# Kernel optimization log

Hardware: AMD Instinct MI355X
Metric: run time of the kernel (lower is better)

Reference implementation:

```python
import jax, jax.numpy as jnp
import numpy as np

# Qwen3.5 GatedDeltaNet dims
B, T, HID = 2, 2048, 2048
HK, HV, DK, DV, KW = 16, 32, 128, 128, 4   # k-heads, v-heads, head dims, conv kernel
R = HV // HK                                # GQA repeat factor = 2
KEY_DIM = HK * DK                           # 2048
VAL_DIM = HV * DV                           # 4096
CONV_DIM = 2 * KEY_DIM + VAL_DIM            # 8192
EPS = 1e-6


def setup_inputs() -> dict:
    key = jax.random.key(0)
    ks = jax.random.split(key, 10)
    w = lambda k, shape, s=0.02: (jax.random.normal(k, shape) * s).astype(jnp.float32)
    A = jax.random.uniform(ks[8], (HV,), minval=1e-3, maxval=16.0)
    return {
        "hidden_states": jax.random.normal(ks[0], (B, T, HID), jnp.float32),
        "W_qkv": w(ks[1], (HID, CONV_DIM)),
        "W_z": w(ks[2], (HID, VAL_DIM)),
        "W_b": w(ks[3], (HID, HV)),
        "W_a": w(ks[4], (HID, HV)),
        "conv_w": w(ks[5], (CONV_DIM, KW), 0.5),   # depthwise causal conv taps
        "dt_bias": jnp.ones((HV,), jnp.float32),
        "A_log": jnp.log(A).astype(jnp.float32),
        "norm_weight": jnp.ones((DV,), jnp.float32),
        "W_out": w(ks[9], (VAL_DIM, HID)),
    }


def _forward(hidden_states, W_qkv, W_z, W_b, W_a, conv_w, dt_bias, A_log, norm_weight, W_out):
    x = hidden_states
    # --- projections ---
    qkv = x @ W_qkv                                    # [B,T,CONV_DIM]
    z = x @ W_z                                        # [B,T,VAL_DIM]
    beta = jax.nn.sigmoid(x @ W_b)                     # [B,T,HV]
    alpha = x @ W_a                                    # [B,T,HV]
    g = -jnp.exp(A_log) * jax.nn.softplus(alpha + dt_bias)  # [B,T,HV] (log-decay <= 0)

    # --- fix_query_key_value_ordering: per-k-head interleaved layout ---
    qkv = qkv.reshape(B, T, HK, 2 * DK + R * DV)
    q, k, v = jnp.split(qkv, [DK, 2 * DK], axis=3)
    mixed = jnp.concatenate([q.reshape(B, T, -1), k.reshape(B, T, -1), v.reshape(B, T, -1)], axis=-1)

    # --- causal depthwise short conv (kernel 4) + SiLU ---
    xp = jnp.pad(mixed, ((0, 0), (KW - 1, 0), (0, 0)))
    conv = sum(conv_w[:, i] * xp[:, i:i + T, :] for i in range(KW))
    conv = jax.nn.silu(conv)

    q, k, v = jnp.split(conv, [KEY_DIM, 2 * KEY_DIM], axis=-1)
    q = q.reshape(B, T, HK, DK)
    k = k.reshape(B, T, HK, DK)
    v = v.reshape(B, T, HV, DV)
    gate = z.reshape(B, T, HV, DV)

    # GQA: repeat q,k heads to match v heads
    q = jnp.repeat(q, R, axis=2)                       # [B,T,HV,DK]
    k = jnp.repeat(k, R, axis=2)

    # l2-norm q,k (use_qk_l2norm_in_kernel=True) and default scale 1/sqrt(DK)
    q = q / jnp.sqrt(jnp.sum(q * q, axis=-1, keepdims=True) + 1e-6)
    k = k / jnp.sqrt(jnp.sum(k * k, axis=-1, keepdims=True) + 1e-6)
    q = q * (DK ** -0.5)

    # --- gated delta rule recurrence (scan over time) ---
    # state S: [B,HV,DK,DV];  S_t = a_t*S_{t-1} + k_t (beta_t*(v_t - (a_t*S_{t-1})^T k_t))^T
    def step(S, inp):
        qt, kt, vt, gt, bt = inp                       # [B,HV,DK],[B,HV,DK],[B,HV,DV],[B,HV],[B,HV]
        S = S * jnp.exp(gt)[:, :, None, None]
        kv = jnp.einsum('bhk,bhkv->bhv', kt, S)
        delta = bt[..., None] * (vt - kv)              # [B,HV,DV]
        S = S + kt[..., None] * delta[:, :, None, :]
        o = jnp.einsum('bhk,bhkv->bhv', qt, S)
        return S, o

    tfirst = lambda a: jnp.moveaxis(a, 1, 0)           # [T,B,...]
    S0 = jnp.zeros((B, HV, DK, DV), q.dtype)
    _, o = jax.lax.scan(step, S0, (tfirst(q), tfirst(k), tfirst(v), tfirst(g), tfirst(beta)))
    o = jnp.moveaxis(o, 0, 1)                          # [B,T,HV,DV]

    # --- gated RMSNorm: rmsnorm(o) * silu(gate) * weight ---
    var = jnp.mean(o * o, axis=-1, keepdims=True)
    o = o * jax.lax.rsqrt(var + EPS)
    o = o * jax.nn.silu(gate)
    o = o * norm_weight

    return o.reshape(B, T, VAL_DIM) @ W_out            # [B,T,HID]


def reference(hidden_states, W_qkv, W_z, W_b, W_a, conv_w, dt_bias, A_log, norm_weight, W_out):
    return _forward(hidden_states, W_qkv, W_z, W_b, W_a, conv_w, dt_bias, A_log, norm_weight, W_out)
```

## Files before the change

kernel.cpp:

```cpp
#include <hip/hip_runtime.h>


#define T_LEN 2048
#define MROWS 4096

typedef __bf16 bf16x8 __attribute__((ext_vector_type(8)));
typedef float f32x4 __attribute__((ext_vector_type(4)));

#define MFMA(a, b, c) __builtin_amdgcn_mfma_f32_16x16x32_bf16((a), (b), (c), 0, 0, 0)

__device__ __forceinline__ unsigned short f2bf(float f) {
  unsigned int u = __float_as_uint(f);
  unsigned int r = (u + 0x7fffu + ((u >> 16) & 1u)) >> 16;
  return (unsigned short)r;
}
__device__ __forceinline__ float bf2f(unsigned short u) {
  return __uint_as_float(((unsigned int)u) << 16);
}
__device__ __forceinline__ void gload_lds16(const void* g, void* l) {
  __builtin_amdgcn_global_load_lds(
      (const __attribute__((address_space(1))) unsigned int*)g,
      (__attribute__((address_space(3))) unsigned int*)l, 16, 0, 0);
}

__global__ __launch_bounds__(256) void f32_to_bf16_vec(const float* __restrict__ src,
                                                       unsigned short* __restrict__ dst,
                                                       int n4) {
  int i = blockIdx.x * 256 + threadIdx.x;
  if (i >= n4) return;
  float4 v = ((const float4*)src)[i];
  ushort4 o;
  o.x = f2bf(v.x); o.y = f2bf(v.y); o.z = f2bf(v.z); o.w = f2bf(v.w);
  ((ushort4*)dst)[i] = o;
}

__global__ __launch_bounds__(256) void transpose_f2b(const float* __restrict__ src,
                                                     unsigned short* __restrict__ dst,
                                                     int R, int C) {
  __shared__ float tile[32][33];
  int tx = threadIdx.x & 31, ty = threadIdx.x >> 5;
  int c0 = blockIdx.x * 32, r0 = blockIdx.y * 32;
  #pragma unroll
  for (int i = ty; i < 32; i += 8)
    tile[i][tx] = src[(size_t)(r0 + i) * C + c0 + tx];
  __syncthreads();
  #pragma unroll
  for (int i = ty; i < 32; i += 8)
    dst[(size_t)(c0 + i) * R + r0 + tx] = f2bf(tile[tx][i]);
}

template <int OUTBF, int BN>
__global__ __launch_bounds__(512, 2) void gemm256(const unsigned short* __restrict__ A, int lda,
                                                  const unsigned short* __restrict__ Bt, int ldb,
                                                  void* __restrict__ Cv, int ldc,
                                                  int M, int N, int K) {
  constexpr int BUFSZ = 16384 + BN * 64;
  constexpr int BISS = BN / 64;
  constexpr int IS = 4 + BISS;
  constexpr int WMv = (BN == 256) ? 2 : 4;
  constexpr int MSUB = 256 / (WMv * 16);
  constexpr int MSPAN = 256 / WMv;

  __shared__ unsigned short lds[2 * BUFSZ];

  const int mtiles = M >> 8;
  const int nwg = gridDim.x;
  const int orig = blockIdx.x;
  const int q = nwg >> 3, r = nwg & 7;
  const int xcd = orig & 7, idx = orig >> 3;
  const int swz = (xcd < r ? xcd * (q + 1) : r * (q + 1) + (xcd - r) * q) + idx;
  const int m0 = (swz % mtiles) * 256;
  const int n0 = (swz / mtiles) * BN;

  const int tid = threadIdx.x, lane = tid & 63, wv = tid >> 6;
  const int wm = (BN == 256) ? (wv >> 2) : (wv >> 1);
  const int wn = (BN == 256) ? (wv & 3) : (wv & 1);
  const int l15 = lane & 15, l4 = lane >> 4;

  f32x4 acc[MSUB][4];
  #pragma unroll
  for (int i = 0; i < MSUB; i++)
    #pragma unroll
    for (int j = 0; j < 4; j++) acc[i][j] = f32x4{0.f, 0.f, 0.f, 0.f};

  const int NT = K >> 6;

  auto STAGE = [&](int kt) {
    unsigned short* base = lds + (kt & 1) * BUFSZ;
    const int k0 = kt << 6;
    #pragma unroll
    for (int is = 0; is < 4; is++) {
      int ow = is * 8192 + wv * 1024;
      int o = ow + lane * 16;
      int row = o >> 7, colB = o & 127;
      int scol = colB ^ ((row & 7) << 4);
      gload_lds16(A + (size_t)(m0 + row) * lda + k0 + (scol >> 1), base + (ow >> 1));
    }
    #pragma unroll
    for (int is = 0; is < BISS; is++) {
      int ow = is * 8192 + wv * 1024;
      int o = ow + lane * 16;
      int row = o >> 7, colB = o & 127;
      int scol = colB ^ ((row & 7) << 4);
      gload_lds16(Bt + (size_t)(n0 + row) * ldb + k0 + (scol >> 1), base + 16384 + (ow >> 1));
    }
  };

  STAGE(0);
  if (NT > 1) STAGE(1);
  if constexpr (IS == 8) asm volatile("s_waitcnt vmcnt(8)" ::: "memory");
  else                   asm volatile("s_waitcnt vmcnt(6)" ::: "memory");
  __builtin_amdgcn_sched_barrier(0);
  __builtin_amdgcn_s_barrier();
  __builtin_amdgcn_sched_barrier(0);

  for (int t = 0; t < NT; t++) {
    const unsigned short* Abuf = lds + (t & 1) * BUFSZ;
    const unsigned short* Bbuf = Abuf + 16384;
    bf16x8 bF[4][2];
    #pragma unroll
    for (int n = 0; n < 4; n++) {
      int rb = wn * 64 + n * 16 + l15;
      int sw = (rb & 7) << 4;
      #pragma unroll
      for (int ks = 0; ks < 2; ks++) {
        int colB = (ks * 32 + l4 * 8) * 2;
        bF[n][ks] = *(const bf16x8*)(Bbuf + rb * 64 + ((colB ^ sw) >> 1));
      }
    }
    __builtin_amdgcn_s_setprio(1);
    #pragma unroll
    for (int m = 0; m < MSUB; m++) {
      int ra = wm * MSPAN + m * 16 + l15;
      int sw = (ra & 7) << 4;
      int c0b = l4 * 16;
      bf16x8 a0 = *(const bf16x8*)(Abuf + ra * 64 + ((c0b ^ sw) >> 1));
      bf16x8 a1 = *(const bf16x8*)(Abuf + ra * 64 + (((64 + c0b) ^ sw) >> 1));
      #pragma unroll
      for (int n = 0; n < 4; n++) {
        acc[m][n] = MFMA(a0, bF[n][0], acc[m][n]);
        acc[m][n] = MFMA(a1, bF[n][1], acc[m][n]);
      }
    }
    __builtin_amdgcn_s_setprio(0);
    __builtin_amdgcn_sched_barrier(0);
    __builtin_amdgcn_s_barrier();
    __builtin_amdgcn_sched_barrier(0);
    if (t + 2 < NT) STAGE(t + 2);
    if (t + 1 < NT) {
      if (t + 2 < NT) {
        if constexpr (IS == 8) asm volatile("s_waitcnt vmcnt(8)" ::: "memory");
        else                   asm volatile("s_waitcnt vmcnt(6)" ::: "memory");
      } else {
        asm volatile("s_waitcnt vmcnt(0)" ::: "memory");
      }
      __builtin_amdgcn_sched_barrier(0);
      __builtin_amdgcn_s_barrier();
      __builtin_amdgcn_sched_barrier(0);
    }
  }

  #pragma unroll
  for (int m = 0; m < MSUB; m++) {
    int grow = m0 + wm * MSPAN + m * 16 + l4 * 4;
    #pragma unroll
    for (int n = 0; n < 4; n++) {
      int gcol = n0 + wn * 64 + n * 16 + l15;
      if (OUTBF) {
        unsigned short* cp = (unsigned short*)Cv + (size_t)grow * ldc + gcol;
        #pragma unroll
        for (int rr = 0; rr < 4; rr++) cp[(size_t)rr * ldc] = f2bf(acc[m][n][rr]);
      } else {
        float* cp = (float*)Cv + (size_t)grow * ldc + gcol;
        #pragma unroll
        for (int rr = 0; rr < 4; rr++) cp[(size_t)rr * ldc] = acc[m][n][rr];
      }
    }
  }
}

template <int OUTBF>
__global__ __launch_bounds__(256) void gemm_bf16(const unsigned short* __restrict__ A, int lda,
                                                 const unsigned short* __restrict__ Bt, int ldb,
                                                 void* __restrict__ Cv, int ldc,
                                                 int M, int N, int K) {
  __shared__ unsigned short As[128 * 64];
  __shared__ unsigned short Bs[128 * 64];
  const int tid = threadIdx.x, lane = tid & 63, wv = tid >> 6;
  const int wr = wv >> 1, wc = wv & 1;
  const int m0 = blockIdx.y * 128, n0 = blockIdx.x * 128;
  const int lrow8 = lane >> 3;
  const int lk8 = (lane & 7) * 8;

  f32x4 acc[4][4];
  #pragma unroll
  for (int i = 0; i < 4; i++)
    #pragma unroll
    for (int j = 0; j < 4; j++) acc[i][j] = f32x4{0.f, 0.f, 0.f, 0.f};

  for (int k0 = 0; k0 < K; k0 += 64) {
    #pragma unroll
    for (int j = 0; j < 4; ++j) {
      int chunk = j * 4 + wv;
      int r = chunk * 8 + lrow8;
      gload_lds16(A + (size_t)(m0 + r) * lda + k0 + lk8, (void*)(As + chunk * 512));
      gload_lds16(Bt + (size_t)(n0 + r) * ldb + k0 + lk8, (void*)(Bs + chunk * 512));
    }
    __syncthreads();
    #pragma unroll
    for (int half = 0; half < 2; ++half) {
      int ko = half * 32 + (lane >> 4) * 8;
      bf16x8 af[4], bfr[4];
      #pragma unroll
      for (int i = 0; i < 4; i++) {
        int ra = wr * 64 + i * 16 + (lane & 15);
        af[i] = *(const bf16x8*)(As + ra * 64 + ko);
        int rb = wc * 64 + i * 16 + (lane & 15);
        bfr[i] = *(const bf16x8*)(Bs + rb * 64 + ko);
      }
      #pragma unroll
      for (int i = 0; i < 4; i++)
        #pragma unroll
        for (int j = 0; j < 4; j++)
          acc[i][j] = MFMA(af[i], bfr[j], acc[i][j]);
    }
    __syncthreads();
  }
  int cr4 = (lane >> 4) * 4;
  int cc = lane & 15;
  #pragma unroll
  for (int i = 0; i < 4; i++) {
    int row = m0 + wr * 64 + i * 16 + cr4;
    #pragma unroll
    for (int j = 0; j < 4; j++) {
      int col = n0 + wc * 64 + j * 16 + cc;
      if (OUTBF) {
        unsigned short* cp = (unsigned short*)Cv + (size_t)row * ldc + col;
        #pragma unroll
        for (int r = 0; r < 4; r++) cp[(size_t)r * ldc] = f2bf(acc[i][j][r]);
      } else {
        float* cp = (float*)Cv + (size_t)row * ldc + col;
        #pragma unroll
        for (int r = 0; r < 4; r++) cp[(size_t)r * ldc] = acc[i][j][r];
      }
    }
  }
}

__global__ __launch_bounds__(256) void beta_g_kernel(const unsigned short* __restrict__ ba,
                                                     const float* __restrict__ A_log,
                                                     const float* __restrict__ dt_bias,
                                                     unsigned short* __restrict__ betab,
                                                     float* __restrict__ g) {
  int i = blockIdx.x * 256 + threadIdx.x;
  int row = i >> 5, hv = i & 31;
  float rb = bf2f(ba[(size_t)row * 128 + hv]);
  float ra = bf2f(ba[(size_t)row * 128 + 32 + hv]);
  betab[i] = f2bf(1.f / (1.f + expf(-rb)));
  float xg = ra + dt_bias[hv];
  float sp = (xg > 20.f) ? xg : log1pf(expf(xg));
  g[i] = -expf(A_log[hv]) * sp;
}

__global__ __launch_bounds__(256) void conv_kernel(const unsigned short* __restrict__ qkv,
                                                   const float* __restrict__ conv_w,
                                                   unsigned short* __restrict__ out) {
  const int seg = blockIdx.x, tt = blockIdx.y, b = blockIdx.z;
  const int tid = threadIdx.x;
  const int c0 = seg * 128;
  const bool isq = seg < 16;
  int scb;
  if (isq) scb = seg * 512;
  else if (seg < 32) scb = (seg - 16) * 512 + 128;
  else scb = ((seg - 32) >> 1) * 512 + 256 + ((seg - 32) & 1) * 128;

  __shared__ unsigned short raw[35][136];
  __shared__ float cw[4][132];

  for (int i = tid; i < 512; i += 256) {
    int cl = i >> 2, tap = i & 3;
    cw[tap][cl] = conv_w[(size_t)(c0 + cl) * 4 + tap];
  }
  const int t0 = tt * 32;
  for (int i = tid; i < 560; i += 256) {
    int row = i >> 4, col = (i & 15) * 8;
    int gt = t0 - 3 + row;
    uint4 v = make_uint4(0u, 0u, 0u, 0u);
    if (gt >= 0) v = *(const uint4*)(qkv + (size_t)(b * T_LEN + gt) * 8192 + scb + col);
    *(uint4*)(&raw[row][col]) = v;
  }
  __syncthreads();
  const int s = tid >> 3, dg = tid & 7;
  union RawU { uint4 v[2]; unsigned short h[16]; };
  RawU u[4];
  #pragma unroll
  for (int i = 0; i < 4; i++) {
    const uint4* p = (const uint4*)&raw[s + i][dg * 16];
    u[i].v[0] = p[0]; u[i].v[1] = p[1];
  }
  float vals[16]; float ss = 0.f;
  #pragma unroll
  for (int j = 0; j < 16; j++) {
    float a = 0.f;
    #pragma unroll
    for (int i = 0; i < 4; i++) a = fmaf(cw[i][dg * 16 + j], bf2f(u[i].h[j]), a);
    a = a / (1.f + expf(-a));
    vals[j] = a; ss += a * a;
  }
  if (seg < 32) {
    ss += __shfl_xor(ss, 1); ss += __shfl_xor(ss, 2); ss += __shfl_xor(ss, 4);
    float sc = rsqrtf(ss + 1e-6f);
    if (isq) sc *= 0.08838834764831845f;
    #pragma unroll
    for (int j = 0; j < 16; j++) vals[j] *= sc;
  }
  union { uint4 v[2]; unsigned short h[16]; } ov;
  #pragma unroll
  for (int j = 0; j < 16; j++) ov.h[j] = f2bf(vals[j]);
  unsigned short* op = out + (size_t)(b * T_LEN + t0 + s) * 8192 + c0 + dg * 16;
  *(uint4*)(op) = ov.v[0];
  *(uint4*)(op + 8) = ov.v[1];
}

__global__ __launch_bounds__(256) void prep_kernel(const unsigned short* __restrict__ conv,
                                                   const float* __restrict__ g,
                                                   const unsigned short* __restrict__ betab,
                                                   unsigned short* __restrict__ M1g,
                                                   unsigned short* __restrict__ M2g,
                                                   unsigned char* __restrict__ vecs) {
  const int c = blockIdx.x, bh = blockIdx.y;
  const int b = bh >> 5, hv = bh & 31, hk = hv >> 1;
  const int bhc = bh * 32 + c;
  const int tid = threadIdx.x, lane = tid & 63, wv = tid >> 6;
  const int r0 = b * T_LEN + c * 64;
  const int l15 = lane & 15, l4 = lane >> 4;

  __shared__ unsigned short Kb[128 * 72];
  __shared__ unsigned short QbX[64 * 136];
  __shared__ unsigned short Lbf[64 * 72];
  __shared__ unsigned short Pb[64 * 72];
  __shared__ unsigned short WT[3 * 16 * 40];
  __shared__ float Gs[64], SCs[64], BLs[64];

  unsigned short* Qb = QbX;
  unsigned short* XTb = QbX;
  unsigned short* Xdrow = QbX + 4608;

  if (wv == 0) {
    float gt = g[(size_t)(r0 + lane) * 32 + hv];
    #pragma unroll
    for (int d = 1; d < 64; d <<= 1) {
      float o = __shfl_up(gt, (unsigned)d, 64);
      if (lane >= d) gt += o;
    }
    float GC = __shfl(gt, 63, 64);
    float lam = expf(gt);
    float beta = bf2f(betab[(size_t)(r0 + lane) * 32 + hv]);
    Gs[lane] = gt;
    SCs[lane] = expf(GC - gt);
    BLs[lane] = beta;
    unsigned short* vb16 = (unsigned short*)(vecs + (size_t)bhc * 272);
    vb16[lane] = f2bf(beta * lam);
    vb16[64 + lane] = f2bf(lam);
    if (lane == 0) *(float*)(vecs + (size_t)bhc * 272 + 256) = expf(GC);
  }
  const unsigned short* Kg = conv + (size_t)r0 * 8192 + 2048 + hk * 128;
  const unsigned short* Qg = conv + (size_t)r0 * 8192 + hk * 128;
  for (int u = tid; u < 1024; u += 256) {
    int row = u >> 4, col = (u & 15) * 8;
    *(uint4*)(&Kb[row * 136 + col]) = *(const uint4*)(Kg + (size_t)row * 8192 + col);
    *(uint4*)(&Qb[row * 136 + col]) = *(const uint4*)(Qg + (size_t)row * 8192 + col);
  }
  __syncthreads();

  {
    f32x4 akk[4], aqk[4];
    #pragma unroll
    for (int st = 0; st < 4; st++) { akk[st] = f32x4{0,0,0,0}; aqk[st] = f32x4{0,0,0,0}; }
    int trow = wv * 16 + l15;
    int klo = l4 * 8;
    #pragma unroll
    for (int ks = 0; ks < 4; ks++) {
      int ko = ks * 32 + klo;
      bf16x8 ak = *(const bf16x8*)(&Kb[trow * 136 + ko]);
      bf16x8 aq = *(const bf16x8*)(&Qb[trow * 136 + ko]);
      #pragma unroll
      for (int st = 0; st < 4; st++) {
        bf16x8 bk = *(const bf16x8*)(&Kb[(st * 16 + l15) * 136 + ko]);
        akk[st] = MFMA(ak, bk, akk[st]);
        aqk[st] = MFMA(aq, bk, aqk[st]);
      }
    }
    int orow = wv * 16 + l4 * 4;
    int oc = l15;
    #pragma unroll
    for (int st = 0; st < 4; st++)
      #pragma unroll
      for (int r = 0; r < 4; r++) {
        int t = orow + r, ssv = st * 16 + oc;
        float e = expf(fminf(Gs[t] - Gs[ssv], 0.f));
        Lbf[t * 72 + ssv] = f2bf((ssv < t) ? BLs[t] * e * akk[st][r] : 0.f);
        Pb[t * 72 + ssv] = f2bf((ssv <= t) ? e * aqk[st][r] : 0.f);
      }
  }
  __syncthreads();

  unsigned short ktv[32];
  {
    int dk = tid >> 1, tb = (tid & 1) * 32;
    #pragma unroll
    for (int i = 0; i < 32; i++)
      ktv[i] = f2bf(bf2f(Kb[(tb + i) * 136 + dk]) * SCs[tb + i]);
    for (int u = tid; u < 896; u += 256) {
      *(uint4*)(&QbX[u * 8]) = make_uint4(0u, 0u, 0u, 0u);
    }
    for (int u = tid; u < 240; u += 256) {
      *(uint4*)(&WT[u * 8]) = make_uint4(0u, 0u, 0u, 0u);
    }
  }
  __syncthreads();

  {
    int dk = tid >> 1, tb = (tid & 1) * 32;
    #pragma unroll
    for (int i = 0; i < 32; i++) Kb[dk * 72 + tb + i] = ktv[i];
  }
  {
    const int w16 = wv * 16;
    const int cc = l15;
    float xr[16];
    #pragma unroll
    for (int t = 0; t < 16; t++) {
      float acc = (cc == t) ? 1.f : 0.f;
      union { uint4 v[2]; unsigned short h[16]; } rw;
      const uint4* p = (const uint4*)(&Lbf[(w16 + t) * 72 + w16]);
      rw.v[0] = p[0]; rw.v[1] = p[1];
      #pragma unroll
      for (int s = 0; s < 16; s++) {
        if (s < t) acc = fmaf(-bf2f(rw.h[s]), xr[s], acc);
      }
      xr[t] = acc;
    }
    if (lane < 16) {
      #pragma unroll
      for (int t = 0; t < 16; t++) {
        unsigned short v = f2bf(xr[t]);
        XTb[(w16 + cc) * 72 + w16 + t] = v;
        Xdrow[wv * 640 + t * 40 + cc] = v;
      }
    }
  }
  __syncthreads();

  if (wv < 3) {
    const int j = wv;
    for (int i = j + 1; i < 4; i++) {
      f32x4 w_ = f32x4{0.f, 0.f, 0.f, 0.f};
      #pragma unroll
      for (int ks = 0; ks < 2; ks++) {
        int so = ks * 32 + l4 * 8;
        bf16x8 af = *(const bf16x8*)(&Lbf[(i * 16 + l15) * 72 + so]);
        bf16x8 bfv = *(const bf16x8*)(&XTb[(j * 16 + l15) * 72 + so]);
        w_ = MFMA(af, bfv, w_);
      }
      #pragma unroll
      for (int r = 0; r < 4; r++)
        WT[j * 640 + l15 * 40 + l4 * 4 + r] = f2bf(-w_[r]);
      f32x4 xij = f32x4{0.f, 0.f, 0.f, 0.f};
      {
        bf16x8 af = *(const bf16x8*)(&Xdrow[i * 640 + l15 * 40 + l4 * 8]);
        bf16x8 bfv = *(const bf16x8*)(&WT[j * 640 + l15 * 40 + l4 * 8]);
        xij = MFMA(af, bfv, xij);
      }
      #pragma unroll
      for (int r = 0; r < 4; r++)
        XTb[(j * 16 + l15) * 72 + i * 16 + l4 * 4 + r] = f2bf(xij[r]);
    }
  }
  __syncthreads();

  for (int tt = wv * 12; tt < wv * 12 + 12; tt++) {
    f32x4 acc = f32x4{0, 0, 0, 0};
    const unsigned short* Abase;
    int mrow, jc;
    if (tt < 16) { mrow = (tt >> 2) * 16; jc = (tt & 3) * 16; Abase = Pb + mrow * 72; }
    else { int i2 = tt - 16; mrow = (i2 >> 2) * 16; jc = (i2 & 3) * 16; Abase = Kb + mrow * 72; }
    #pragma unroll
    for (int ks = 0; ks < 2; ks++) {
      int so = ks * 32 + l4 * 8;
      bf16x8 af = *(const bf16x8*)(Abase + l15 * 72 + so);
      bf16x8 bfv = *(const bf16x8*)(&XTb[(jc + l15) * 72 + so]);
      acc = MFMA(af, bfv, acc);
    }
    int ro = mrow + l4 * 4, co = jc + l15;
    if (tt < 16) {
      #pragma unroll
      for (int r = 0; r < 4; r++)
        M1g[(size_t)bhc * 4096 + (ro + r) * 64 + co] = f2bf(acc[r]);
    } else {
      #pragma unroll
      for (int r = 0; r < 4; r++)
        M2g[(size_t)bhc * 8192 + (ro + r) * 64 + co] = f2bf(acc[r]);
    }
  }
}

__global__ __launch_bounds__(256) void seq_kernel(unsigned short* __restrict__ conv,
                                                  const unsigned short* __restrict__ M1g,
                                                  const unsigned short* __restrict__ M2g,
                                                  const unsigned char* __restrict__ vecs,
                                                  const unsigned short* __restrict__ betab) {
  const int dvs = blockIdx.x, bh = blockIdx.y;
  const int b = bh >> 5, hv = bh & 31, hk = hv >> 1;
  const int dv0 = dvs * 16;
  const int tid = threadIdx.x, lane = tid & 63, wv = tid >> 6;

  __shared__ unsigned short Kb[64 * 136], Qb[64 * 136];
  __shared__ float Sf[128 * 20];
  __shared__ unsigned short S0T[16 * 136];
  __shared__ unsigned short rhsT[16 * 72];

  for (int i = tid; i < 128 * 20; i += 256) Sf[i] = 0.f;
  for (int i = tid; i < 16 * 136; i += 256) S0T[i] = 0;
  __syncthreads();

  const int l15 = lane & 15, l4 = lane >> 4;
  const int trt = wv * 16;

  for (int c = 0; c < 32; c++) {
    const int r0 = b * T_LEN + c * 64;
    const int bhc = bh * 32 + c;
    const unsigned char* vb = vecs + (size_t)bhc * 272;
    const unsigned short* vb16 = (const unsigned short*)vb;
    #pragma unroll
    for (int j = 0; j < 4; j++) {
      int u = j * 256 + tid;
      int row = u >> 4, col = (u & 15) * 8;
      uint4 kv = *(const uint4*)(conv + (size_t)(r0 + row) * 8192 + 2048 + hk * 128 + col);
      uint4 qv = *(const uint4*)(conv + (size_t)(r0 + row) * 8192 + hk * 128 + col);
      *(uint4*)(&Kb[row * 136 + col]) = kv;
      float lam = bf2f(vb16[64 + row]);
      union { uint4 u4; unsigned short h[8]; } qq; qq.u4 = qv;
      #pragma unroll
      for (int e = 0; e < 8; e++) qq.h[e] = f2bf(bf2f(qq.h[e]) * lam);
      *(uint4*)(&Qb[row * 136 + col]) = qq.u4;
    }
    __syncthreads();
    {
      f32x4 acc = f32x4{0, 0, 0, 0};
      #pragma unroll
      for (int ks = 0; ks < 4; ks++) {
        int ko = ks * 32 + l4 * 8;
        bf16x8 af = *(const bf16x8*)(&Kb[(trt + l15) * 136 + ko]);
        bf16x8 bfv = *(const bf16x8*)(&S0T[l15 * 136 + ko]);
        acc = MFMA(af, bfv, acc);
      }
      #pragma unroll
      for (int r = 0; r < 4; r++) {
        int tl = trt + l4 * 4 + r;
        int t = r0 + tl;
        float beta = bf2f(betab[(size_t)t * 32 + hv]);
        float bl = bf2f(vb16[tl]);
        float vv = bf2f(conv[(size_t)t * 8192 + 4096 + hv * 128 + dv0 + l15]);
        rhsT[l15 * 72 + tl] = f2bf(beta * vv - bl * acc[r]);
      }
    }
    __syncthreads();
    {
      f32x4 acc = f32x4{0, 0, 0, 0};
      const unsigned short* m1b = M1g + (size_t)bhc * 4096;
      #pragma unroll
      for (int ks = 0; ks < 2; ks++) {
        int so = ks * 32 + l4 * 8;
        union { uint4 u4; bf16x8 h; } af;
        af.u4 = *(const uint4*)(m1b + (trt + l15) * 64 + so);
        bf16x8 bfv = *(const bf16x8*)(&rhsT[l15 * 72 + so]);
        acc = MFMA(af.h, bfv, acc);
      }
      #pragma unroll
      for (int ks = 0; ks < 4; ks++) {
        int ko = ks * 32 + l4 * 8;
        bf16x8 af = *(const bf16x8*)(&Qb[(trt + l15) * 136 + ko]);
        bf16x8 bfv = *(const bf16x8*)(&S0T[l15 * 136 + ko]);
        acc = MFMA(af, bfv, acc);
      }
      #pragma unroll
      for (int r = 0; r < 4; r++) {
        int t = r0 + trt + l4 * 4 + r;
        conv[(size_t)t * 8192 + 4096 + hv * 128 + dv0 + l15] = f2bf(acc[r]);
      }
    }
    {
      float lamC = *(const float*)(vb + 256);
      f32x4 sacc[2];
      const unsigned short* m2b = M2g + (size_t)bhc * 8192;
      #pragma unroll
      for (int dkt = 0; dkt < 2; dkt++) {
        int dkb = (wv * 2 + dkt) * 16;
        f32x4 a;
        #pragma unroll
        for (int r = 0; r < 4; r++) a[r] = lamC * Sf[(dkb + l4 * 4 + r) * 20 + l15];
        #pragma unroll
        for (int ks = 0; ks < 2; ks++) {
          int so = ks * 32 + l4 * 8;
          union { uint4 u4; bf16x8 h; } af;
          af.u4 = *(const uint4*)(m2b + (dkb + l15) * 64 + so);
          bf16x8 bfv = *(const bf16x8*)(&rhsT[l15 * 72 + so]);
          a = MFMA(af.h, bfv, a);
        }
        sacc[dkt] = a;
      }
      __syncthreads();
      #pragma unroll
      for (int dkt = 0; dkt < 2; dkt++) {
        int dkb = (wv * 2 + dkt) * 16;
        #pragma unroll
        for (int r = 0; r < 4; r++) {
          int dk = dkb + l4 * 4 + r;
          Sf[dk * 20 + l15] = sacc[dkt][r];
          S0T[l15 * 136 + dk] = f2bf(sacc[dkt][r]);
        }
      }
    }
    __syncthreads();
  }
}

__global__ __launch_bounds__(256) void rmsgate_kernel(unsigned short* __restrict__ conv,
                                                      const unsigned short* __restrict__ zg,
                                                      const float* __restrict__ nw) {
  int wid = blockIdx.x * 4 + (threadIdx.x >> 6);
  int lane = threadIdx.x & 63;
  int row = wid >> 5, hv = wid & 31;
  unsigned short* op = conv + (size_t)row * 8192 + 4096 + hv * 128;
  float o0 = bf2f(op[lane]), o1 = bf2f(op[64 + lane]);
  float ss = o0 * o0 + o1 * o1;
  #pragma unroll
  for (int m = 1; m < 64; m <<= 1) ss += __shfl_xor(ss, m);
  float r = rsqrtf(ss * (1.f / 128.f) + 1e-6f);
  const unsigned short* zp = zg + (size_t)row * 4096 + hv * 128;
  float g0 = bf2f(zp[lane]), g1 = bf2f(zp[64 + lane]);
  g0 = g0 / (1.f + expf(-g0));
  g1 = g1 / (1.f + expf(-g1));
  op[lane] = f2bf(o0 * r * g0 * nw[lane]);
  op[64 + lane] = f2bf(o1 * r * g1 * nw[64 + lane]);
}

extern "C" void kernel_launch(void* const* d_in, const int* in_sizes, int n_in,
                              void* d_out, int out_size, void* d_ws, size_t ws_size,
                              hipStream_t stream) {
  (void)in_sizes; (void)n_in; (void)out_size;
  const float* x       = (const float*)d_in[0];
  const float* W_qkv   = (const float*)d_in[1];
  const float* W_z     = (const float*)d_in[2];
  const float* W_b     = (const float*)d_in[3];
  const float* W_a     = (const float*)d_in[4];
  const float* conv_w  = (const float*)d_in[5];
  const float* dt_bias = (const float*)d_in[6];
  const float* A_log   = (const float*)d_in[7];
  const float* nw      = (const float*)d_in[8];
  const float* W_out   = (const float*)d_in[9];
  float* out = (float*)d_out;

  const size_t NEED = 169115648ULL;
  if (ws_size < NEED) return;

  char* ws = (char*)d_ws;
  unsigned short* qkv_bf = (unsigned short*)(ws + 0);
  unsigned short* M1g    = (unsigned short*)(ws + 0);
  unsigned short* M2g    = (unsigned short*)(ws + 16777216);
  unsigned short* WoutT  = (unsigned short*)(ws + 0);
  unsigned short* zg     = (unsigned short*)(ws + 67108864);
  unsigned short* WzT    = (unsigned short*)(ws + 100663296);
  unsigned short* x_bf   = (unsigned short*)(ws + 100663296 + 16777216);
  unsigned short* WqkvT  = (unsigned short*)(ws + 100663296 + 33554432);
  unsigned short* WbaT   = (unsigned short*)(ws + 100663296 + 33554432);
  unsigned short* ba     = (unsigned short*)(ws + 100663296 + 34078720);
  unsigned short* convb  = (unsigned short*)(ws + 100663296);
  unsigned short* betab  = (unsigned short*)(ws + 167772160);
  float* gbuf            = (float*)(ws + 168034304);
  unsigned char* vecs    = (unsigned char*)(ws + 168558592);

  const int M = MROWS;

  f32_to_bf16_vec<<<(M * 2048 / 4) / 256, 256, 0, stream>>>(x, x_bf, M * 2048 / 4);
  transpose_f2b<<<dim3(8192 / 32, 2048 / 32), 256, 0, stream>>>(W_qkv, WqkvT, 2048, 8192);
  transpose_f2b<<<dim3(4096 / 32, 2048 / 32), 256, 0, stream>>>(W_z, WzT, 2048, 4096);

  gemm256<1, 256><<<512, 512, 0, stream>>>(x_bf, 2048, WqkvT, 2048, qkv_bf, 8192, M, 8192, 2048);

  transpose_f2b<<<dim3(1, 64), 256, 0, stream>>>(W_b, WbaT, 2048, 32);
  transpose_f2b<<<dim3(1, 64), 256, 0, stream>>>(W_a, WbaT + (size_t)32 * 2048, 2048, 32);

  gemm256<1, 256><<<256, 512, 0, stream>>>(x_bf, 2048, WzT, 2048, zg, 4096, M, 4096, 2048);
  gemm_bf16<1><<<dim3(1, M / 128), 256, 0, stream>>>(x_bf, 2048, WbaT, 2048, ba, 128, M, 128, 2048);

  beta_g_kernel<<<(M * 32) / 256, 256, 0, stream>>>(ba, A_log, dt_bias, betab, gbuf);

  conv_kernel<<<dim3(64, 64, 2), 256, 0, stream>>>(qkv_bf, conv_w, convb);

  prep_kernel<<<dim3(32, 64), 256, 0, stream>>>(convb, gbuf, betab, M1g, M2g, vecs);

  seq_kernel<<<dim3(8, 64), 256, 0, stream>>>(convb, M1g, M2g, vecs, betab);

  rmsgate_kernel<<<32768, 256, 0, stream>>>(convb, zg, nw);

  transpose_f2b<<<dim3(2048 / 32, 4096 / 32), 256, 0, stream>>>(W_out, WoutT, 4096, 2048);
  gemm256<0, 128><<<256, 512, 0, stream>>>(convb + 4096, 8192, WoutT, 4096, out, 2048, M, 2048, 4096);
}
```

Measured before the change: 627.0 us.

## Pack GEMM operands into k-chunked layout and use 128x128 tile GEMM for input projections

Replaces the row-major bf16 conversion and transposes with packing kernels that store x and the weights in a k-chunk-major layout (8 bf16 per 16-byte chunk). A new 128x128-tile GEMM with double-buffered direct-to-LDS loads and XCD-aware block swizzling reads these contiguous chunks for the qkv, z and beta/alpha projections, replacing both the 256-tile GEMM and the simple GEMM. The aim is contiguous, conflict-free LDS fragment reads and better occupancy. The trade-off is smaller tiles, so each operand is loaded from global memory more times, and the W_b/W_a packing leaves columns 64..127 of WbaC unwritten (only 64 of the 128 packed columns are filled).

```diff
diff --git a/kernel.cpp b/kernel.cpp
--- a/kernel.cpp
+++ b/kernel.cpp
@@ -23,15 +23,48 @@
       (__attribute__((address_space(3))) unsigned int*)l, 16, 0, 0);
 }
 
-__global__ __launch_bounds__(256) void f32_to_bf16_vec(const float* __restrict__ src,
-                                                       unsigned short* __restrict__ dst,
-                                                       int n4) {
-  int i = blockIdx.x * 256 + threadIdx.x;
-  if (i >= n4) return;
-  float4 v = ((const float4*)src)[i];
-  ushort4 o;
-  o.x = f2bf(v.x); o.y = f2bf(v.y); o.z = f2bf(v.z); o.w = f2bf(v.w);
-  ((ushort4*)dst)[i] = o;
+__global__ __launch_bounds__(256) void pack_x(const float* __restrict__ src,
+                                              unsigned short* __restrict__ dst) {
+  __shared__ float t[64][33];
+  const int tid = threadIdx.x;
+  const int kt = blockIdx.x * 32, rt = blockIdx.y * 64;
+  for (int u = tid; u < 512; u += 256) {
+    int row = u >> 3, f4 = u & 7;
+    float4 v = *(const float4*)(src + (size_t)(rt + row) * 2048 + kt + f4 * 4);
+    t[row][f4 * 4 + 0] = v.x; t[row][f4 * 4 + 1] = v.y;
+    t[row][f4 * 4 + 2] = v.z; t[row][f4 * 4 + 3] = v.w;
+  }
+  __syncthreads();
+  int row = tid & 63, kcl = tid >> 6;
+  union { uint4 u4; unsigned short h[8]; } o;
+  #pragma unroll
+  for (int e = 0; e < 8; e++) o.h[e] = f2bf(t[row][kcl * 8 + e]);
+  *(uint4*)(dst + ((size_t)((kt >> 3) + kcl) * 4096 + rt + row) * 8) = o.u4;
+}
+
+__global__ __launch_bounds__(256) void pack_w(const float* __restrict__ src,
+                                              unsigned short* __restrict__ dst,
+                                              int C, int dstN, int coff) {
+  __shared__ float t[32][65];
+  const int tid = threadIdx.x;
+  const int kt = blockIdx.y * 32, ct = blockIdx.x * 64;
+  for (int u = tid; u < 512; u += 256) {
+    int kl = u >> 4, f4 = u & 15;
+    int c = ct + f4 * 4;
+    if (c < C) {
+      float4 v = *(const float4*)(src + (size_t)(kt + kl) * C + c);
+      t[kl][f4 * 4 + 0] = v.x; t[kl][f4 * 4 + 1] = v.y;
+      t[kl][f4 * 4 + 2] = v.z; t[kl][f4 * 4 + 3] = v.w;
+    }
+  }
+  __syncthreads();
+  int col = tid & 63, kcl = tid >> 6;
+  if (ct + col < C) {
+    union { uint4 u4; unsigned short h[8]; } o;
+    #pragma unroll
+    for (int e = 0; e < 8; e++) o.h[e] = f2bf(t[kcl * 8 + e][col]);
+    *(uint4*)(dst + ((size_t)((kt >> 3) + kcl) * dstN + coff + ct + col) * 8) = o.u4;
+  }
 }
 
 __global__ __launch_bounds__(256) void transpose_f2b(const float* __restrict__ src,
@@ -47,6 +80,108 @@
   #pragma unroll
   for (int i = ty; i < 32; i += 8)
     dst[(size_t)(c0 + i) * R + r0 + tx] = f2bf(tile[tx][i]);
+}
+
+template <int OUTBF>
+__global__ __launch_bounds__(256, 4) void gemm256c(const unsigned short* __restrict__ Ac, int Arows,
+                                                   const unsigned short* __restrict__ Bc, int Bcols,
+                                                   void* __restrict__ Cv, int ldc,
+                                                   int M, int N, int K) {
+  constexpr int BUFSZ = 8192;
+  __shared__ unsigned short lds[2 * BUFSZ];
+
+  const int mtiles = M >> 7;
+  const int nwg = gridDim.x;
+  const int orig = blockIdx.x;
+  const int q = nwg >> 3, r = nwg & 7;
+  const int xcd = orig & 7, idx = orig >> 3;
+  const int swz = (xcd < r ? xcd * (q + 1) : r * (q + 1) + (xcd - r) * q) + idx;
+  const int m0 = (swz % mtiles) * 128;
+  const int n0 = (swz / mtiles) * 128;
+
+  const int tid = threadIdx.x, lane = tid & 63, wv = tid >> 6;
+  const int wm = wv >> 1, wn = wv & 1;
+  const int l15 = lane & 15, l4 = lane >> 4;
+
+  f32x4 acc[4][4];
+  #pragma unroll
+  for (int i = 0; i < 4; i++)
+    #pragma unroll
+    for (int j = 0; j < 4; j++) acc[i][j] = f32x4{0.f, 0.f, 0.f, 0.f};
+
+  const int NT = K >> 5;
+
+  auto STAGE = [&](int kt) {
+    unsigned short* base = lds + (kt & 1) * BUFSZ;
+    const int kb = kt << 2;
+    #pragma unroll
+    for (int is = 0; is < 2; is++) {
+      int c = is * 256 + tid;
+      int kc = c >> 7, row = c & 127;
+      gload_lds16(Ac + ((size_t)(kb + kc) * Arows + m0 + row) * 8,
+                  base + is * 2048 + wv * 512);
+    }
+    #pragma unroll
+    for (int is = 0; is < 2; is++) {
+      int c = is * 256 + tid;
+      int kc = c >> 7, col = c & 127;
+      gload_lds16(Bc + ((size_t)(kb + kc) * Bcols + n0 + col) * 8,
+                  base + 4096 + is * 2048 + wv * 512);
+    }
+  };
+
+  STAGE(0);
+  if (NT > 1) STAGE(1);
+  asm volatile("s_waitcnt vmcnt(4)" ::: "memory");
+  __builtin_amdgcn_sched_barrier(0);
+  __builtin_amdgcn_s_barrier();
+  __builtin_amdgcn_sched_barrier(0);
+
+  for (int t = 0; t < NT; t++) {
+    const unsigned short* Abuf = lds + (t & 1) * BUFSZ;
+    const unsigned short* Bbuf = Abuf + 4096;
+    bf16x8 bF[4];
+    #pragma unroll
+    for (int n = 0; n < 4; n++)
+      bF[n] = *(const bf16x8*)(Bbuf + (size_t)(l4 * 128 + wn * 64 + n * 16 + l15) * 8);
+    __builtin_amdgcn_s_setprio(1);
+    #pragma unroll
+    for (int m = 0; m < 4; m++) {
+      bf16x8 aF = *(const bf16x8*)(Abuf + (size_t)(l4 * 128 + wm * 64 + m * 16 + l15) * 8);
+      #pragma unroll
+      for (int n = 0; n < 4; n++) acc[m][n] = MFMA(aF, bF[n], acc[m][n]);
+    }
+    __builtin_amdgcn_s_setprio(0);
+    __builtin_amdgcn_sched_barrier(0);
+    __builtin_amdgcn_s_barrier();
+    __builtin_amdgcn_sched_barrier(0);
+    if (t + 2 < NT) STAGE(t + 2);
+    if (t + 1 < NT) {
+      if (t + 2 < NT) asm volatile("s_waitcnt vmcnt(4)" ::: "memory");
+      else            asm volatile("s_waitcnt vmcnt(0)" ::: "memory");
+      __builtin_amdgcn_sched_barrier(0);
+      __builtin_amdgcn_s_barrier();
+      __builtin_amdgcn_sched_barrier(0);
+    }
+  }
+
+  #pragma unroll
+  for (int m = 0; m < 4; m++) {
+    int grow = m0 + wm * 64 + m * 16 + l4 * 4;
+    #pragma unroll
+    for (int n = 0; n < 4; n++) {
+      int gcol = n0 + wn * 64 + n * 16 + l15;
+      if (OUTBF) {
+        unsigned short* cp = (unsigned short*)Cv + (size_t)grow * ldc + gcol;
+        #pragma unroll
+        for (int rr = 0; rr < 4; rr++) cp[(size_t)rr * ldc] = f2bf(acc[m][n][rr]);
+      } else {
+        float* cp = (float*)Cv + (size_t)grow * ldc + gcol;
+        #pragma unroll
+        for (int rr = 0; rr < 4; rr++) cp[(size_t)rr * ldc] = acc[m][n][rr];
+      }
+    }
+  }
 }
 
 template <int OUTBF, int BN>
@@ -174,74 +309,6 @@
         float* cp = (float*)Cv + (size_t)grow * ldc + gcol;
         #pragma unroll
         for (int rr = 0; rr < 4; rr++) cp[(size_t)rr * ldc] = acc[m][n][rr];
-      }
-    }
-  }
-}
-
-template <int OUTBF>
-__global__ __launch_bounds__(256) void gemm_bf16(const unsigned short* __restrict__ A, int lda,
-                                                 const unsigned short* __restrict__ Bt, int ldb,
-                                                 void* __restrict__ Cv, int ldc,
-                                                 int M, int N, int K) {
-  __shared__ unsigned short As[128 * 64];
-  __shared__ unsigned short Bs[128 * 64];
-  const int tid = threadIdx.x, lane = tid & 63, wv = tid >> 6;
-  const int wr = wv >> 1, wc = wv & 1;
-  const int m0 = blockIdx.y * 128, n0 = blockIdx.x * 128;
-  const int lrow8 = lane >> 3;
-  const int lk8 = (lane & 7) * 8;
-
-  f32x4 acc[4][4];
-  #pragma unroll
-  for (int i = 0; i < 4; i++)
-    #pragma unroll
-    for (int j = 0; j < 4; j++) acc[i][j] = f32x4{0.f, 0.f, 0.f, 0.f};
-
-  for (int k0 = 0; k0 < K; k0 += 64) {
-    #pragma unroll
-    for (int j = 0; j < 4; ++j) {
-      int chunk = j * 4 + wv;
-      int r = chunk * 8 + lrow8;
-      gload_lds16(A + (size_t)(m0 + r) * lda + k0 + lk8, (void*)(As + chunk * 512));
-      gload_lds16(Bt + (size_t)(n0 + r) * ldb + k0 + lk8, (void*)(Bs + chunk * 512));
-    }
-    __syncthreads();
-    #pragma unroll
-    for (int half = 0; half < 2; ++half) {
-      int ko = half * 32 + (lane >> 4) * 8;
-      bf16x8 af[4], bfr[4];
-      #pragma unroll
-      for (int i = 0; i < 4; i++) {
-        int ra = wr * 64 + i * 16 + (lane & 15);
-        af[i] = *(const bf16x8*)(As + ra * 64 + ko);
-        int rb = wc * 64 + i * 16 + (lane & 15);
-        bfr[i] = *(const bf16x8*)(Bs + rb * 64 + ko);
-      }
-      #pragma unroll
-      for (int i = 0; i < 4; i++)
-        #pragma unroll
-        for (int j = 0; j < 4; j++)
-          acc[i][j] = MFMA(af[i], bfr[j], acc[i][j]);
-    }
-    __syncthreads();
-  }
-  int cr4 = (lane >> 4) * 4;
-  int cc = lane & 15;
-  #pragma unroll
-  for (int i = 0; i < 4; i++) {
-    int row = m0 + wr * 64 + i * 16 + cr4;
-    #pragma unroll
-    for (int j = 0; j < 4; j++) {
-      int col = n0 + wc * 64 + j * 16 + cc;
-      if (OUTBF) {
-        unsigned short* cp = (unsigned short*)Cv + (size_t)row * ldc + col;
-        #pragma unroll
-        for (int r = 0; r < 4; r++) cp[(size_t)r * ldc] = f2bf(acc[i][j][r]);
-      } else {
-        float* cp = (float*)Cv + (size_t)row * ldc + col;
-        #pragma unroll
-        for (int r = 0; r < 4; r++) cp[(size_t)r * ldc] = acc[i][j][r];
       }
     }
   }
@@ -671,10 +738,10 @@
   unsigned short* M2g    = (unsigned short*)(ws + 16777216);
   unsigned short* WoutT  = (unsigned short*)(ws + 0);
   unsigned short* zg     = (unsigned short*)(ws + 67108864);
-  unsigned short* WzT    = (unsigned short*)(ws + 100663296);
-  unsigned short* x_bf   = (unsigned short*)(ws + 100663296 + 16777216);
-  unsigned short* WqkvT  = (unsigned short*)(ws + 100663296 + 33554432);
-  unsigned short* WbaT   = (unsigned short*)(ws + 100663296 + 33554432);
+  unsigned short* WzC    = (unsigned short*)(ws + 100663296);
+  unsigned short* Ac     = (unsigned short*)(ws + 100663296 + 16777216);
+  unsigned short* WqkvC  = (unsigned short*)(ws + 100663296 + 33554432);
+  unsigned short* WbaC   = (unsigned short*)(ws + 100663296 + 33554432);
   unsigned short* ba     = (unsigned short*)(ws + 100663296 + 34078720);
   unsigned short* convb  = (unsigned short*)(ws + 100663296);
   unsigned short* betab  = (unsigned short*)(ws + 167772160);
@@ -683,17 +750,17 @@
 
   const int M = MROWS;
 
-  f32_to_bf16_vec<<<(M * 2048 / 4) / 256, 256, 0, stream>>>(x, x_bf, M * 2048 / 4);
-  transpose_f2b<<<dim3(8192 / 32, 2048 / 32), 256, 0, stream>>>(W_qkv, WqkvT, 2048, 8192);
-  transpose_f2b<<<dim3(4096 / 32, 2048 / 32), 256, 0, stream>>>(W_z, WzT, 2048, 4096);
-
-  gemm256<1, 256><<<512, 512, 0, stream>>>(x_bf, 2048, WqkvT, 2048, qkv_bf, 8192, M, 8192, 2048);
-
-  transpose_f2b<<<dim3(1, 64), 256, 0, stream>>>(W_b, WbaT, 2048, 32);
-  transpose_f2b<<<dim3(1, 64), 256, 0, stream>>>(W_a, WbaT + (size_t)32 * 2048, 2048, 32);
-
-  gemm256<1, 256><<<256, 512, 0, stream>>>(x_bf, 2048, WzT, 2048, zg, 4096, M, 4096, 2048);
-  gemm_bf16<1><<<dim3(1, M / 128), 256, 0, stream>>>(x_bf, 2048, WbaT, 2048, ba, 128, M, 128, 2048);
+  pack_x<<<dim3(64, 64), 256, 0, stream>>>(x, Ac);
+  pack_w<<<dim3(128, 64), 256, 0, stream>>>(W_qkv, WqkvC, 8192, 8192, 0);
+  pack_w<<<dim3(64, 64), 256, 0, stream>>>(W_z, WzC, 4096, 4096, 0);
+
+  gemm256c<1><<<2048, 256, 0, stream>>>(Ac, 4096, WqkvC, 8192, qkv_bf, 8192, M, 8192, 2048);
+
+  pack_w<<<dim3(1, 64), 256, 0, stream>>>(W_b, WbaC, 32, 128, 0);
+  pack_w<<<dim3(1, 64), 256, 0, stream>>>(W_a, WbaC, 32, 128, 32);
+
+  gemm256c<1><<<1024, 256, 0, stream>>>(Ac, 4096, WzC, 4096, zg, 4096, M, 4096, 2048);
+  gemm256c<1><<<32, 256, 0, stream>>>(Ac, 4096, WbaC, 128, ba, 128, M, 128, 2048);
 
   beta_g_kernel<<<(M * 32) / 256, 256, 0, stream>>>(ba, A_log, dt_bias, betab, gbuf);
 
```

After: 655.1 us. 4.5% more time.

## Add 8-phase pipelined 256x256 GEMM for QKV and Z projections

Applied to the files above, without the earlier changes.

Introduces a new bf16 GEMM kernel that splits each K-step into four quadrant compute phases, interleaving half-tile async global-to-LDS loads and LDS fragment reads with MFMA work under explicit barriers and priority hints. It replaces the previous gemm256 kernel for the two large input projections. The goal is to hide memory and LDS latency behind MFMA work. In exchange it adds many barriers per iteration and relies on hand-tuned vmcnt waits, which is fragile if the load ordering changes.

```diff
diff --git a/kernel.cpp b/kernel.cpp
--- a/kernel.cpp
+++ b/kernel.cpp
@@ -47,6 +47,146 @@
   #pragma unroll
   for (int i = ty; i < 32; i += 8)
     dst[(size_t)(c0 + i) * R + r0 + tx] = f2bf(tile[tx][i]);
+}
+
+template <int OUTBF>
+__global__ __launch_bounds__(512, 2) void gemm8p(const unsigned short* __restrict__ A, int lda,
+                                                 const unsigned short* __restrict__ Bt, int ldb,
+                                                 void* __restrict__ Cv, int ldc,
+                                                 int M, int N, int K) {
+  __shared__ unsigned short lds[65536];
+
+  const int mtiles = M >> 8;
+  const int nwg = gridDim.x, orig = blockIdx.x;
+  const int q = nwg >> 3, r = nwg & 7;
+  const int xcd = orig & 7, idx = orig >> 3;
+  const int swz = (xcd < r ? xcd * (q + 1) : r * (q + 1) + (xcd - r) * q) + idx;
+  const int m0 = (swz % mtiles) * 256;
+  const int n0 = (swz / mtiles) * 256;
+
+  const int tid = threadIdx.x, lane = tid & 63, wv = tid >> 6;
+  const int wm = wv >> 2, wn = wv & 3;
+  const int l15 = lane & 15, l4 = lane >> 4;
+
+  f32x4 acc[8][4];
+  #pragma unroll
+  for (int i = 0; i < 8; i++)
+    #pragma unroll
+    for (int j = 0; j < 4; j++) acc[i][j] = f32x4{0.f, 0.f, 0.f, 0.f};
+
+  const int NT = K >> 6;
+
+  auto SHALF = [&](int t, int op, int h) {
+    unsigned short* base = lds + (t & 1) * 32768 + op * 16384 + h * 8192;
+    const unsigned short* G = op ? Bt : A;
+    const int ld = op ? ldb : lda;
+    const int r0g = (op ? n0 : m0) + h * 128;
+    const int k0 = t << 6;
+    #pragma unroll
+    for (int is = 0; is < 2; is++) {
+      int ow = is * 8192 + wv * 1024;
+      int o = ow + lane * 16;
+      int row = o >> 7, colB = o & 127;
+      int scol = colB ^ ((row & 7) << 4);
+      gload_lds16(G + (size_t)(r0g + row) * ld + k0 + (scol >> 1), base + (ow >> 1));
+    }
+  };
+
+  bf16x8 aF[4][2], bF[2][2];
+  auto RD_A = [&](int t, int qm) {
+    const unsigned short* base = lds + (t & 1) * 32768 + qm * 8192;
+    #pragma unroll
+    for (int mi = 0; mi < 4; mi++) {
+      int ra = wm * 64 + mi * 16 + l15;
+      int sw = (ra & 7) << 4;
+      #pragma unroll
+      for (int kh = 0; kh < 2; kh++) {
+        int colB = kh * 64 + l4 * 16;
+        aF[mi][kh] = *(const bf16x8*)(base + ra * 64 + ((colB ^ sw) >> 1));
+      }
+    }
+  };
+  auto RD_B = [&](int t, int qn) {
+    const unsigned short* base = lds + (t & 1) * 32768 + 16384 + qn * 8192;
+    #pragma unroll
+    for (int ni = 0; ni < 2; ni++) {
+      int rb = wn * 32 + ni * 16 + l15;
+      int sw = (rb & 7) << 4;
+      #pragma unroll
+      for (int kh = 0; kh < 2; kh++) {
+        int colB = kh * 64 + l4 * 16;
+        bF[ni][kh] = *(const bf16x8*)(base + rb * 64 + ((colB ^ sw) >> 1));
+      }
+    }
+  };
+  auto COMPUTE = [&](int qm, int qn) {
+    __builtin_amdgcn_s_setprio(1);
+    #pragma unroll
+    for (int mi = 0; mi < 4; mi++)
+      #pragma unroll
+      for (int ni = 0; ni < 2; ni++)
+        #pragma unroll
+        for (int kh = 0; kh < 2; kh++)
+          acc[qm * 4 + mi][qn * 2 + ni] =
+              MFMA(aF[mi][kh], bF[ni][kh], acc[qm * 4 + mi][qn * 2 + ni]);
+    __builtin_amdgcn_s_setprio(0);
+  };
+  auto SBAR = [&]() {
+    __builtin_amdgcn_sched_barrier(0);
+    __builtin_amdgcn_s_barrier();
+    __builtin_amdgcn_sched_barrier(0);
+  };
+
+  SHALF(0, 0, 0); SHALF(0, 1, 0); SHALF(0, 0, 1); SHALF(0, 1, 1);
+  if (NT > 1) { SHALF(1, 1, 0); SHALF(1, 0, 1); }
+  asm volatile("s_waitcnt vmcnt(4)" ::: "memory");
+  SBAR();
+
+  for (int t = 0; t < NT; t++) {
+    if (t > 0) {
+      if (t >= NT - 2) asm volatile("s_waitcnt vmcnt(0)" ::: "memory");
+      else             asm volatile("s_waitcnt vmcnt(4)" ::: "memory");
+      SBAR();
+    }
+    RD_A(t, 0); RD_B(t, 0);
+    if (t + 1 < NT) SHALF(t + 1, 1, 1);
+    SBAR();
+    COMPUTE(0, 0);
+    SBAR();
+    RD_A(t, 1);
+    if (t + 1 < NT) SHALF(t + 1, 0, 0);
+    SBAR();
+    COMPUTE(1, 0);
+    SBAR();
+    RD_B(t, 1);
+    if (t + 2 < NT) SHALF(t + 2, 1, 0);
+    SBAR();
+    COMPUTE(1, 1);
+    SBAR();
+    RD_A(t, 0);
+    if (t + 2 < NT) SHALF(t + 2, 0, 1);
+    SBAR();
+    COMPUTE(0, 1);
+    SBAR();
+  }
+
+  #pragma unroll
+  for (int i = 0; i < 8; i++) {
+    int grow = m0 + (i >> 2) * 128 + wm * 64 + (i & 3) * 16 + l4 * 4;
+    #pragma unroll
+    for (int j = 0; j < 4; j++) {
+      int gcol = n0 + (j >> 1) * 128 + wn * 32 + (j & 1) * 16 + l15;
+      if (OUTBF) {
+        unsigned short* cp = (unsigned short*)Cv + (size_t)grow * ldc + gcol;
+        #pragma unroll
+        for (int rr = 0; rr < 4; rr++) cp[(size_t)rr * ldc] = f2bf(acc[i][j][rr]);
+      } else {
+        float* cp = (float*)Cv + (size_t)grow * ldc + gcol;
+        #pragma unroll
+        for (int rr = 0; rr < 4; rr++) cp[(size_t)rr * ldc] = acc[i][j][rr];
+      }
+    }
+  }
 }
 
 template <int OUTBF, int BN>
@@ -687,12 +827,12 @@
   transpose_f2b<<<dim3(8192 / 32, 2048 / 32), 256, 0, stream>>>(W_qkv, WqkvT, 2048, 8192);
   transpose_f2b<<<dim3(4096 / 32, 2048 / 32), 256, 0, stream>>>(W_z, WzT, 2048, 4096);
 
-  gemm256<1, 256><<<512, 512, 0, stream>>>(x_bf, 2048, WqkvT, 2048, qkv_bf, 8192, M, 8192, 2048);
+  gemm8p<1><<<512, 512, 0, stream>>>(x_bf, 2048, WqkvT, 2048, qkv_bf, 8192, M, 8192, 2048);
 
   transpose_f2b<<<dim3(1, 64), 256, 0, stream>>>(W_b, WbaT, 2048, 32);
   transpose_f2b<<<dim3(1, 64), 256, 0, stream>>>(W_a, WbaT + (size_t)32 * 2048, 2048, 32);
 
-  gemm256<1, 256><<<256, 512, 0, stream>>>(x_bf, 2048, WzT, 2048, zg, 4096, M, 4096, 2048);
+  gemm8p<1><<<256, 512, 0, stream>>>(x_bf, 2048, WzT, 2048, zg, 4096, M, 4096, 2048);
   gemm_bf16<1><<<dim3(1, M / 128), 256, 0, stream>>>(x_bf, 2048, WbaT, 2048, ba, 128, M, 128, 2048);
 
   beta_g_kernel<<<(M * 32) / 256, 256, 0, stream>>>(ba, A_log, dt_bias, betab, gbuf);
```

Measured after the change: 638.6 us. About the same (+1.9%).
